# Kernel optimization log

Hardware: AMD Instinct MI355X
Metric: run time of the kernel (lower is better)

## Reference

```python
import jax, jax.numpy as jnp
import numpy as np

B, S, D, H, E = 2, 2048, 1024, 4096, 8


def setup_inputs() -> dict:
    key = jax.random.key(0)
    k0, k1, k2, k3 = jax.random.split(key, 4)
    x = jax.random.normal(k0, (B, S, D), dtype=jnp.float32)
    router_w = jax.random.normal(k1, (E, D), dtype=jnp.float32) * 0.02   # Top2Router Linear weight [E, D]
    w1 = jax.random.normal(k2, (E, D, H), dtype=jnp.float32) * 0.02      # stacked fc1 weights (transposed: x @ w1[e])
    w2 = jax.random.normal(k3, (E, H, D), dtype=jnp.float32) * 0.02      # stacked fc2 weights
    return {"x": x, "router_w": router_w, "w1": w1, "w2": w2}


def reference(x, router_w, w1, w2):
    # x: [B, S, D] -> flatten tokens. Single-rank EP: all-to-all is identity,
    # microbatch split is a pure overlap trick, per-token math unchanged.
    b, s, d = x.shape
    e = router_w.shape[0]
    xf = x.reshape(-1, d)                                     # [T, D]
    # Top-2 router with renormalized gate weights
    probs = jax.nn.softmax(xf @ router_w.T, axis=-1)          # [T, E]
    topv, topi = jax.lax.top_k(probs, 2)                      # [T, 2]
    topv = topv / (topv.sum(axis=-1, keepdims=True) + 1e-9)
    # Combine weights per expert: cw[t,e] = sum_k topv[t,k] * [topi[t,k]==e]
    cw = (jax.nn.one_hot(topi, e, dtype=xf.dtype) * topv[..., None]).sum(axis=1)  # [T, E]
    # Expert MLPs (dense-over-experts reference for the grouped GEMM)
    h = jax.nn.gelu(jnp.einsum('td,edh->teh', xf, w1), approximate=False)  # [T, E, H]
    y = jnp.einsum('teh,ehd->ted', h, w2)                                   # [T, E, D]
    out = jnp.einsum('te,ted->td', cw, y)                                   # weighted combine (scatter-add equiv.)
    return out.reshape(b, s, d)
```

## Files before the change

kernel.cpp:

```cpp
#include <hip/hip_runtime.h>

#define T_TOK 4096
#define DIM   1024
#define HID   4096
#define NEXP  8
#define MAXROWS 9216

typedef unsigned short u16;
typedef __attribute__((ext_vector_type(8))) short short8;
typedef __attribute__((ext_vector_type(4))) float f32x4;
typedef __attribute__((ext_vector_type(4))) unsigned short u16x4;
typedef __attribute__((ext_vector_type(8))) unsigned short u16x8;

typedef __attribute__((address_space(3))) unsigned int lds_uint;
typedef const __attribute__((address_space(1))) unsigned int gbl_uint;

__device__ __forceinline__ u16 f2bf(float f) {
    union { float f; unsigned int u; } v; v.f = f;
    unsigned int r = v.u + 0x7fffu + ((v.u >> 16) & 1u);
    return (u16)(r >> 16);
}

__device__ __forceinline__ float gelu_f(float v) {
    float u = 1.5957691216f * (v + 0.044715f * v * v * v);
    float s = 1.0f / (1.0f + __expf(-u));
    return v * s;
}

__global__ __launch_bounds__(256)
void transpose_cast2(const float* __restrict__ w1, u16* __restrict__ w1t,
                     const float* __restrict__ w2, u16* __restrict__ w2t,
                     int* __restrict__ counts) {
    int b = blockIdx.x;
    if (b == 0 && threadIdx.x < NEXP) counts[threadIdx.x] = 0;
    const float* in; u16* out; int R, C, bx, by, e;
    if (b < 8192) {
        e = b >> 10; int t = b & 1023; bx = t & 63; by = t >> 6;
        in = w1; out = w1t; R = DIM; C = HID;
    } else {
        b -= 8192;
        e = b >> 10; int t = b & 1023; bx = t & 15; by = t >> 4;
        in = w2; out = w2t; R = HID; C = DIM;
    }
    __shared__ u16 t[64 * 68];
    size_t mo = (size_t)e * DIM * HID;
    const float* ip = in + mo;
    u16* op = out + mo;
    int c0 = bx * 64, r0 = by * 64;
    int tid = threadIdx.x;
#pragma unroll
    for (int j = 0; j < 4; ++j) {
        int id = tid + 256 * j;
        int r = id >> 4, cc = id & 15;
        f32x4 v = *(const f32x4*)(ip + (size_t)(r0 + r) * C + c0 + 4 * cc);
        u16x4 w; w.x = f2bf(v.x); w.y = f2bf(v.y); w.z = f2bf(v.z); w.w = f2bf(v.w);
        *(u16x4*)(t + r * 68 + 4 * cc) = w;
    }
    __syncthreads();
#pragma unroll
    for (int j = 0; j < 4; ++j) {
        int id = tid + 256 * j;
        int c = id >> 4, rj = id & 15;
        u16x4 o;
        o.x = t[(4 * rj + 0) * 68 + c];
        o.y = t[(4 * rj + 1) * 68 + c];
        o.z = t[(4 * rj + 2) * 68 + c];
        o.w = t[(4 * rj + 3) * 68 + c];
        *(u16x4*)(op + (size_t)(c0 + c) * R + r0 + 4 * rj) = o;
    }
}

__global__ __launch_bounds__(256)
void router_k(const float* __restrict__ x, const float* __restrict__ rw,
              int* __restrict__ counts, int* __restrict__ tE,
              int* __restrict__ tS, float* __restrict__ tG) {
    int wave = threadIdx.x >> 6, lane = threadIdx.x & 63;
    int t = blockIdx.x * 4 + wave;
    const float* xr = x + (size_t)t * DIM;
    float xv[16];
#pragma unroll
    for (int i = 0; i < 16; ++i) xv[i] = xr[lane + 64*i];
    float lg[NEXP];
#pragma unroll
    for (int e = 0; e < NEXP; ++e) {
        const float* wr_ = rw + e * DIM;
        float a = 0.f;
#pragma unroll
        for (int i = 0; i < 16; ++i) a += xv[i] * wr_[lane + 64*i];
        lg[e] = a;
    }
#pragma unroll
    for (int off = 32; off > 0; off >>= 1)
#pragma unroll
        for (int e = 0; e < NEXP; ++e) lg[e] += __shfl_xor(lg[e], off, 64);
    if (lane == 0) {
        float mx = lg[0];
        for (int e = 1; e < NEXP; ++e) mx = fmaxf(mx, lg[e]);
        float p[NEXP], s = 0.f;
        for (int e = 0; e < NEXP; ++e) { p[e] = expf(lg[e] - mx); s += p[e]; }
        float inv_s = 1.f / s;
        for (int e = 0; e < NEXP; ++e) p[e] *= inv_s;
        int i0 = 0;
        for (int e = 1; e < NEXP; ++e) if (p[e] > p[i0]) i0 = e;
        int i1 = (i0 == 0) ? 1 : 0;
        for (int e = 0; e < NEXP; ++e) if (e != i0 && p[e] > p[i1]) i1 = e;
        float v0 = p[i0], v1 = p[i1];
        float inv = 1.f / (v0 + v1 + 1e-9f);
        int s0 = atomicAdd(&counts[i0], 1);
        int s1 = atomicAdd(&counts[i1], 1);
        tE[2*t] = i0;  tE[2*t+1] = i1;
        tS[2*t] = s0;  tS[2*t+1] = s1;
        tG[2*t] = v0 * inv;  tG[2*t+1] = v1 * inv;
    }
}

__device__ __forceinline__ int pbase_of(const int* __restrict__ counts, int e) {
    int pb = 0;
#pragma unroll
    for (int i = 0; i < NEXP; ++i) {
        int pad = ((counts[i] + 127) >> 7) << 7;
        pb += (i < e) ? pad : 0;
    }
    return pb;
}

__global__ __launch_bounds__(256)
void gather_k(const float* __restrict__ x, const int* __restrict__ tE,
              const int* __restrict__ tS, const int* __restrict__ counts,
              u16* __restrict__ xg) {
    int a = blockIdx.x;
    int t = a >> 1, k = a & 1;
    int e = tE[2*t + k];
    int row = pbase_of(counts, e) + tS[2*t + k];
    const f32x4* xr = (const f32x4*)(x + (size_t)t * DIM);
    u16x4* o = (u16x4*)(xg + (size_t)row * DIM);
    int i = threadIdx.x;
    f32x4 v = xr[i];
    u16x4 r; r.x = f2bf(v.x); r.y = f2bf(v.y); r.z = f2bf(v.z); r.w = f2bf(v.w);
    o[i] = r;
}

template<int K, int KSPLIT, bool GELU, typename OutT>
__global__ __launch_bounds__(256)
void gemm_bt(const u16* __restrict__ A, const u16* __restrict__ BtAll,
             OutT* __restrict__ C, const int* __restrict__ counts,
             int N, size_t cstride) {
    int e  = blockIdx.z / KSPLIT;
    int ks = blockIdx.z % KSPLIT;
    int cnt = counts[e];
    int mt = blockIdx.y;
    if (mt * 128 >= cnt) return;
    int row0 = pbase_of(counts, e) + mt * 128;
    const u16* Bt = BtAll + (size_t)e * N * K;
    OutT* Cp = C + (size_t)ks * cstride;
    int col0 = blockIdx.x * 128;
    const int kb0 = ks * (K / KSPLIT);
    constexpr int KITER = K / KSPLIT / 64;

    __shared__ __align__(16) u16 smem[128 * 128];
    u16* As = smem;
    u16* Bs = smem + 128 * 64;

    int tid = threadIdx.x;
    int lane = tid & 63;
    int w = tid >> 6;
    int quad = lane >> 4, m16 = lane & 15;
    int wr = (w >> 1) * 64, wc = (w & 1) * 64;
    int rsub = lane >> 3;
    int kch  = lane & 7;
    int kchs = kch ^ rsub;

    const u16* ga[4];
    const u16* gb[4];
#pragma unroll
    for (int i = 0; i < 4; ++i) {
        int r = (w * 4 + i) * 8 + rsub;
        ga[i] = A  + (size_t)(row0 + r) * K + kb0 + kchs * 8;
        gb[i] = Bt + (size_t)(col0 + r) * K + kb0 + kchs * 8;
    }
    int sw = m16 & 7;
    const u16* aP0 = As + (wr + m16) * 64 + ((quad       ^ sw) << 3);
    const u16* aP1 = As + (wr + m16) * 64 + (((4 + quad) ^ sw) << 3);
    const u16* bP0 = Bs + (wc + m16) * 64 + ((quad       ^ sw) << 3);
    const u16* bP1 = Bs + (wc + m16) * 64 + (((4 + quad) ^ sw) << 3);

    f32x4 acc[4][4] = {};

    for (int kit = 0; kit < KITER; ++kit) {
#pragma unroll
        for (int i = 0; i < 4; ++i) {
            int grp = w * 4 + i;
            __builtin_amdgcn_global_load_lds((gbl_uint*)ga[i], (lds_uint*)(As + grp * 512), 16, 0, 0);
            __builtin_amdgcn_global_load_lds((gbl_uint*)gb[i], (lds_uint*)(Bs + grp * 512), 16, 0, 0);
            ga[i] += 64; gb[i] += 64;
        }
        __syncthreads();
        {
            short8 af[4], bfr[4];
#pragma unroll
            for (int mi = 0; mi < 4; ++mi) af[mi]  = *(const short8*)(aP0 + mi * 1024);
#pragma unroll
            for (int ni = 0; ni < 4; ++ni) bfr[ni] = *(const short8*)(bP0 + ni * 1024);
#pragma unroll
            for (int mi = 0; mi < 4; ++mi)
#pragma unroll
                for (int ni = 0; ni < 4; ++ni)
                    acc[mi][ni] = __builtin_amdgcn_mfma_f32_16x16x32_bf16(af[mi], bfr[ni], acc[mi][ni], 0, 0, 0);
#pragma unroll
            for (int mi = 0; mi < 4; ++mi) af[mi]  = *(const short8*)(aP1 + mi * 1024);
#pragma unroll
            for (int ni = 0; ni < 4; ++ni) bfr[ni] = *(const short8*)(bP1 + ni * 1024);
#pragma unroll
            for (int mi = 0; mi < 4; ++mi)
#pragma unroll
                for (int ni = 0; ni < 4; ++ni)
                    acc[mi][ni] = __builtin_amdgcn_mfma_f32_16x16x32_bf16(af[mi], bfr[ni], acc[mi][ni], 0, 0, 0);
        }
        __syncthreads();
    }

    if (GELU) {
#pragma unroll
        for (int mi = 0; mi < 4; ++mi) {
#pragma unroll
            for (int r = 0; r < 4; ++r) {
                int row = wr + mi * 16 + quad * 4 + r;
#pragma unroll
                for (int ni = 0; ni < 4; ++ni) {
                    int col = wc + ni * 16 + m16;
                    int c16 = col >> 3, w8 = col & 7;
                    smem[row * 128 + (((c16 ^ (row & 15)) << 3) | w8)] = f2bf(gelu_f(acc[mi][ni][r]));
                }
            }
        }
        __syncthreads();
        int row_b = tid >> 4, c16_b = tid & 15;
        const u16* ls = smem + row_b * 128 + (((c16_b ^ (row_b & 15)) << 3));
        u16* gp = (u16*)Cp + (size_t)(row0 + row_b) * N + col0 + c16_b * 8;
#pragma unroll
        for (int j = 0; j < 8; ++j) {
            *(u16x8*)gp = *(const u16x8*)ls;
            ls += 16 * 128;
            gp += (size_t)16 * N;
        }
    } else {
        float* gp = (float*)Cp + (size_t)(row0 + wr + quad * 4) * N + col0 + wc + m16;
#pragma unroll
        for (int mi = 0; mi < 4; ++mi)
#pragma unroll
            for (int r = 0; r < 4; ++r) {
                float* rp = gp + (size_t)(mi * 16 + r) * N;
#pragma unroll
                for (int ni = 0; ni < 4; ++ni)
                    rp[ni * 16] = acc[mi][ni][r];
            }
    }
}

__global__ __launch_bounds__(256)
void combine_k(const float* __restrict__ p0, const float* __restrict__ p1,
               const int* __restrict__ tE, const int* __restrict__ tS,
               const float* __restrict__ tG, const int* __restrict__ counts,
               float* __restrict__ out) {
    int t = blockIdx.x;
    int e0 = tE[2*t], e1 = tE[2*t+1];
    int r0 = pbase_of(counts, e0) + tS[2*t];
    int r1 = pbase_of(counts, e1) + tS[2*t+1];
    float g0 = tG[2*t], g1 = tG[2*t+1];
    int i = threadIdx.x;
    f32x4 a0 = ((const f32x4*)(p0 + (size_t)r0 * DIM))[i];
    f32x4 b0 = ((const f32x4*)(p1 + (size_t)r0 * DIM))[i];
    f32x4 a1 = ((const f32x4*)(p0 + (size_t)r1 * DIM))[i];
    f32x4 b1 = ((const f32x4*)(p1 + (size_t)r1 * DIM))[i];
    f32x4* o = (f32x4*)(out + (size_t)t * DIM);
    o[i] = g0 * (a0 + b0) + g1 * (a1 + b1);
}

extern "C" void kernel_launch(void* const* d_in, const int* in_sizes, int n_in,
                              void* d_out, int out_size, void* d_ws, size_t ws_size,
                              hipStream_t stream) {
    const float* x  = (const float*)d_in[0];
    const float* rw = (const float*)d_in[1];
    const float* w1 = (const float*)d_in[2];
    const float* w2 = (const float*)d_in[3];
    float* out = (float*)d_out;

    char* ws = (char*)d_ws;
    u16* w1t = (u16*)(ws + 0);
    u16* xg  = (u16*)(ws + 67108864ull);
    u16* w2t = (u16*)(ws + 85983232ull);
    u16* hb  = (u16*)(ws + 153092096ull);
    float* p0 = (float*)(ws + 0);
    float* p1 = (float*)(ws + 37748736ull);
    int* ctrl   = (int*)(ws + 228589568ull);
    int* counts = ctrl;
    int* tE     = ctrl + 32;
    int* tS     = ctrl + 32 + 8192;
    float* tG   = (float*)(ctrl + 32 + 16384);

    transpose_cast2<<<16384, 256, 0, stream>>>(w1, w1t, w2, w2t, counts);
    router_k<<<T_TOK / 4, 256, 0, stream>>>(x, rw, counts, tE, tS, tG);
    gather_k<<<T_TOK * 2, 256, 0, stream>>>(x, tE, tS, counts, xg);
    gemm_bt<DIM, 1, true, u16><<<dim3(HID / 128, 32, NEXP), 256, 0, stream>>>(
        xg, w1t, hb, counts, HID, 0);
    gemm_bt<HID, 2, false, float><<<dim3(DIM / 128, 32, NEXP * 2), 256, 0, stream>>>(
        hb, w2t, p0, counts, DIM, (size_t)MAXROWS * DIM);
    combine_k<<<T_TOK, 256, 0, stream>>>(p0, p1, tE, tS, tG, counts, out);
}
```

Baseline: 671.5 us.

## Use 256x256 double-buffered 8-wave GEMM tiles and larger transpose tiles

Grows the grouped GEMM block tile from 128x128 to 256x256 with 512 threads. It double-buffers LDS so the next K-slab loads while MFMAs run, staged with barriers and s_setprio. Partial expert tiles are handled with row clamping and masked stores. The weight transpose-cast kernel moves to 128x128 tiles with 8-wide stores. The aim is more data reuse per LDS load and load/compute overlap, at the cost of more wasted work on partial tiles and 128KB of LDS per block, which limits occupancy.

Result: slower. 698.7 us (+4.1%).

```diff
diff --git a/kernel.cpp b/kernel.cpp
--- a/kernel.cpp
+++ b/kernel.cpp
@@ -9,6 +9,7 @@
 typedef unsigned short u16;
 typedef __attribute__((ext_vector_type(8))) short short8;
 typedef __attribute__((ext_vector_type(4))) float f32x4;
+typedef __attribute__((ext_vector_type(2))) unsigned short u16x2;
 typedef __attribute__((ext_vector_type(4))) unsigned short u16x4;
 typedef __attribute__((ext_vector_type(8))) unsigned short u16x8;
 
@@ -34,39 +35,39 @@
     int b = blockIdx.x;
     if (b == 0 && threadIdx.x < NEXP) counts[threadIdx.x] = 0;
     const float* in; u16* out; int R, C, bx, by, e;
-    if (b < 8192) {
-        e = b >> 10; int t = b & 1023; bx = t & 63; by = t >> 6;
+    if (b < 2048) {
+        e = b >> 8; int t = b & 255; bx = t & 31; by = t >> 5;
         in = w1; out = w1t; R = DIM; C = HID;
     } else {
-        b -= 8192;
-        e = b >> 10; int t = b & 1023; bx = t & 15; by = t >> 4;
+        b -= 2048;
+        e = b >> 8; int t = b & 255; bx = t & 7; by = t >> 3;
         in = w2; out = w2t; R = HID; C = DIM;
     }
-    __shared__ u16 t[64 * 68];
+    __shared__ u16 tl[128 * 130];
     size_t mo = (size_t)e * DIM * HID;
     const float* ip = in + mo;
     u16* op = out + mo;
-    int c0 = bx * 64, r0 = by * 64;
+    int c0 = bx * 128, r0 = by * 128;
     int tid = threadIdx.x;
 #pragma unroll
-    for (int j = 0; j < 4; ++j) {
+    for (int j = 0; j < 16; ++j) {
         int id = tid + 256 * j;
-        int r = id >> 4, cc = id & 15;
-        f32x4 v = *(const f32x4*)(ip + (size_t)(r0 + r) * C + c0 + 4 * cc);
-        u16x4 w; w.x = f2bf(v.x); w.y = f2bf(v.y); w.z = f2bf(v.z); w.w = f2bf(v.w);
-        *(u16x4*)(t + r * 68 + 4 * cc) = w;
+        int r = id >> 5, cg = id & 31;
+        f32x4 v = *(const f32x4*)(ip + (size_t)(r0 + r) * C + c0 + 4 * cg);
+        u16x2 wa; wa.x = f2bf(v.x); wa.y = f2bf(v.y);
+        u16x2 wb; wb.x = f2bf(v.z); wb.y = f2bf(v.w);
+        *(u16x2*)(tl + r * 130 + 4 * cg)     = wa;
+        *(u16x2*)(tl + r * 130 + 4 * cg + 2) = wb;
     }
     __syncthreads();
 #pragma unroll
-    for (int j = 0; j < 4; ++j) {
+    for (int j = 0; j < 8; ++j) {
         int id = tid + 256 * j;
-        int c = id >> 4, rj = id & 15;
-        u16x4 o;
-        o.x = t[(4 * rj + 0) * 68 + c];
-        o.y = t[(4 * rj + 1) * 68 + c];
-        o.z = t[(4 * rj + 2) * 68 + c];
-        o.w = t[(4 * rj + 3) * 68 + c];
-        *(u16x4*)(op + (size_t)(c0 + c) * R + r0 + 4 * rj) = o;
+        int c = id >> 4, ch = id & 15;
+        u16x8 o;
+#pragma unroll
+        for (int k = 0; k < 8; ++k) o[k] = tl[(ch * 8 + k) * 130 + c];
+        *(u16x8*)(op + (size_t)(c0 + c) * R + r0 + ch * 8) = o;
     }
 }
 
@@ -141,7 +142,7 @@
 }
 
 template<int K, int KSPLIT, bool GELU, typename OutT>
-__global__ __launch_bounds__(256)
+__global__ __launch_bounds__(512, 2)
 void gemm_bt(const u16* __restrict__ A, const u16* __restrict__ BtAll,
              OutT* __restrict__ C, const int* __restrict__ counts,
              int N, size_t cstride) {
@@ -149,23 +150,22 @@
     int ks = blockIdx.z % KSPLIT;
     int cnt = counts[e];
     int mt = blockIdx.y;
-    if (mt * 128 >= cnt) return;
-    int row0 = pbase_of(counts, e) + mt * 128;
+    if (mt * 256 >= cnt) return;
+    int row0 = pbase_of(counts, e) + mt * 256;
+    int limit = cnt - mt * 256;
     const u16* Bt = BtAll + (size_t)e * N * K;
     OutT* Cp = C + (size_t)ks * cstride;
-    int col0 = blockIdx.x * 128;
+    int col0 = blockIdx.x * 256;
     const int kb0 = ks * (K / KSPLIT);
-    constexpr int KITER = K / KSPLIT / 64;
-
-    __shared__ __align__(16) u16 smem[128 * 128];
-    u16* As = smem;
-    u16* Bs = smem + 128 * 64;
+    constexpr int NT = K / KSPLIT / 64;
+
+    __shared__ __align__(16) u16 smem[65536];
 
     int tid = threadIdx.x;
     int lane = tid & 63;
     int w = tid >> 6;
     int quad = lane >> 4, m16 = lane & 15;
-    int wr = (w >> 1) * 64, wc = (w & 1) * 64;
+    int wr = (w >> 2) * 128, wc = (w & 3) * 64;
     int rsub = lane >> 3;
     int kch  = lane & 7;
     int kchs = kch ^ rsub;
@@ -174,85 +174,151 @@
     const u16* gb[4];
 #pragma unroll
     for (int i = 0; i < 4; ++i) {
-        int r = (w * 4 + i) * 8 + rsub;
-        ga[i] = A  + (size_t)(row0 + r) * K + kb0 + kchs * 8;
-        gb[i] = Bt + (size_t)(col0 + r) * K + kb0 + kchs * 8;
+        int g = (w << 2) + i;
+        int ra = row0 + g * 8 + rsub;
+        if (ra > MAXROWS - 1) ra = MAXROWS - 1;
+        ga[i] = A  + (size_t)ra * K + kb0 + kchs * 8;
+        gb[i] = Bt + (size_t)(col0 + g * 8 + rsub) * K + kb0 + kchs * 8;
     }
     int sw = m16 & 7;
-    const u16* aP0 = As + (wr + m16) * 64 + ((quad       ^ sw) << 3);
-    const u16* aP1 = As + (wr + m16) * 64 + (((4 + quad) ^ sw) << 3);
-    const u16* bP0 = Bs + (wc + m16) * 64 + ((quad       ^ sw) << 3);
-    const u16* bP1 = Bs + (wc + m16) * 64 + (((4 + quad) ^ sw) << 3);
-
-    f32x4 acc[4][4] = {};
-
-    for (int kit = 0; kit < KITER; ++kit) {
-#pragma unroll
-        for (int i = 0; i < 4; ++i) {
-            int grp = w * 4 + i;
-            __builtin_amdgcn_global_load_lds((gbl_uint*)ga[i], (lds_uint*)(As + grp * 512), 16, 0, 0);
-            __builtin_amdgcn_global_load_lds((gbl_uint*)gb[i], (lds_uint*)(Bs + grp * 512), 16, 0, 0);
-            ga[i] += 64; gb[i] += 64;
-        }
-        __syncthreads();
-        {
-            short8 af[4], bfr[4];
-#pragma unroll
-            for (int mi = 0; mi < 4; ++mi) af[mi]  = *(const short8*)(aP0 + mi * 1024);
-#pragma unroll
-            for (int ni = 0; ni < 4; ++ni) bfr[ni] = *(const short8*)(bP0 + ni * 1024);
-#pragma unroll
-            for (int mi = 0; mi < 4; ++mi)
-#pragma unroll
-                for (int ni = 0; ni < 4; ++ni)
-                    acc[mi][ni] = __builtin_amdgcn_mfma_f32_16x16x32_bf16(af[mi], bfr[ni], acc[mi][ni], 0, 0, 0);
-#pragma unroll
-            for (int mi = 0; mi < 4; ++mi) af[mi]  = *(const short8*)(aP1 + mi * 1024);
-#pragma unroll
-            for (int ni = 0; ni < 4; ++ni) bfr[ni] = *(const short8*)(bP1 + ni * 1024);
-#pragma unroll
-            for (int mi = 0; mi < 4; ++mi)
-#pragma unroll
-                for (int ni = 0; ni < 4; ++ni)
-                    acc[mi][ni] = __builtin_amdgcn_mfma_f32_16x16x32_bf16(af[mi], bfr[ni], acc[mi][ni], 0, 0, 0);
-        }
-        __syncthreads();
+    const int aoff = (wr + m16) * 64;
+    const int boff = (wc + m16) * 64;
+    const int c0lo = (quad ^ sw) << 3;
+    const int c0hi = ((4 + quad) ^ sw) << 3;
+
+    f32x4 acc[8][4] = {};
+
+#pragma unroll
+    for (int i = 0; i < 4; ++i) {
+        int g = (w << 2) + i;
+        __builtin_amdgcn_global_load_lds((gbl_uint*)ga[i], (lds_uint*)(smem + g * 512), 16, 0, 0);
+        __builtin_amdgcn_global_load_lds((gbl_uint*)gb[i], (lds_uint*)(smem + 32768 + g * 512), 16, 0, 0);
+        ga[i] += 64; gb[i] += 64;
+    }
+    asm volatile("s_waitcnt vmcnt(0)" ::: "memory");
+    __builtin_amdgcn_s_barrier();
+
+#pragma unroll 2
+    for (int t = 0; t < NT; ++t) {
+        const u16* Ab = smem + (t & 1) * 16384;
+        const u16* Bb = smem + 32768 + (t & 1) * 16384;
+        short8 a0[4], a1[4], b0[4], b1[4];
+        if (t + 1 < NT) {
+#pragma unroll
+            for (int i = 0; i < 4; ++i) {
+                int g = (w << 2) + i;
+                __builtin_amdgcn_global_load_lds((gbl_uint*)ga[i],
+                    (lds_uint*)(smem + ((t + 1) & 1) * 16384 + g * 512), 16, 0, 0);
+                __builtin_amdgcn_global_load_lds((gbl_uint*)gb[i],
+                    (lds_uint*)(smem + 32768 + ((t + 1) & 1) * 16384 + g * 512), 16, 0, 0);
+                ga[i] += 64; gb[i] += 64;
+            }
+        }
+#pragma unroll
+        for (int m = 0; m < 4; ++m) {
+            a0[m] = *(const short8*)(Ab + aoff + m * 1024 + c0lo);
+            a1[m] = *(const short8*)(Ab + aoff + m * 1024 + c0hi);
+        }
+#pragma unroll
+        for (int n = 0; n < 2; ++n) {
+            b0[n] = *(const short8*)(Bb + boff + n * 1024 + c0lo);
+            b1[n] = *(const short8*)(Bb + boff + n * 1024 + c0hi);
+        }
+        __builtin_amdgcn_s_barrier();
+        asm volatile("s_waitcnt lgkmcnt(0)" ::: "memory");
+        __builtin_amdgcn_s_setprio(1);
+#pragma unroll
+        for (int m = 0; m < 4; ++m)
+#pragma unroll
+            for (int n = 0; n < 2; ++n) {
+                acc[m][n] = __builtin_amdgcn_mfma_f32_16x16x32_bf16(a0[m], b0[n], acc[m][n], 0, 0, 0);
+                acc[m][n] = __builtin_amdgcn_mfma_f32_16x16x32_bf16(a1[m], b1[n], acc[m][n], 0, 0, 0);
+            }
+        __builtin_amdgcn_s_setprio(0);
+        __builtin_amdgcn_s_barrier();
+#pragma unroll
+        for (int n = 2; n < 4; ++n) {
+            b0[n] = *(const short8*)(Bb + boff + n * 1024 + c0lo);
+            b1[n] = *(const short8*)(Bb + boff + n * 1024 + c0hi);
+        }
+        __builtin_amdgcn_s_barrier();
+        asm volatile("s_waitcnt lgkmcnt(0)" ::: "memory");
+        __builtin_amdgcn_s_setprio(1);
+#pragma unroll
+        for (int m = 0; m < 4; ++m)
+#pragma unroll
+            for (int n = 2; n < 4; ++n) {
+                acc[m][n] = __builtin_amdgcn_mfma_f32_16x16x32_bf16(a0[m], b0[n], acc[m][n], 0, 0, 0);
+                acc[m][n] = __builtin_amdgcn_mfma_f32_16x16x32_bf16(a1[m], b1[n], acc[m][n], 0, 0, 0);
+            }
+        __builtin_amdgcn_s_setprio(0);
+        __builtin_amdgcn_s_barrier();
+#pragma unroll
+        for (int m = 0; m < 4; ++m) {
+            a0[m] = *(const short8*)(Ab + aoff + (4 + m) * 1024 + c0lo);
+            a1[m] = *(const short8*)(Ab + aoff + (4 + m) * 1024 + c0hi);
+        }
+        __builtin_amdgcn_s_barrier();
+        asm volatile("s_waitcnt lgkmcnt(0)" ::: "memory");
+        __builtin_amdgcn_s_setprio(1);
+#pragma unroll
+        for (int m = 0; m < 4; ++m)
+#pragma unroll
+            for (int n = 2; n < 4; ++n) {
+                acc[4 + m][n] = __builtin_amdgcn_mfma_f32_16x16x32_bf16(a0[m], b0[n], acc[4 + m][n], 0, 0, 0);
+                acc[4 + m][n] = __builtin_amdgcn_mfma_f32_16x16x32_bf16(a1[m], b1[n], acc[4 + m][n], 0, 0, 0);
+            }
+        __builtin_amdgcn_s_setprio(0);
+        __builtin_amdgcn_s_barrier();
+        __builtin_amdgcn_s_setprio(1);
+#pragma unroll
+        for (int m = 0; m < 4; ++m)
+#pragma unroll
+            for (int n = 0; n < 2; ++n) {
+                acc[4 + m][n] = __builtin_amdgcn_mfma_f32_16x16x32_bf16(a0[m], b0[n], acc[4 + m][n], 0, 0, 0);
+                acc[4 + m][n] = __builtin_amdgcn_mfma_f32_16x16x32_bf16(a1[m], b1[n], acc[4 + m][n], 0, 0, 0);
+            }
+        __builtin_amdgcn_s_setprio(0);
+        asm volatile("s_waitcnt vmcnt(0)" ::: "memory");
+        __builtin_amdgcn_s_barrier();
     }
 
     if (GELU) {
 #pragma unroll
-        for (int mi = 0; mi < 4; ++mi) {
+        for (int mi = 0; mi < 8; ++mi) {
 #pragma unroll
             for (int r = 0; r < 4; ++r) {
                 int row = wr + mi * 16 + quad * 4 + r;
 #pragma unroll
                 for (int ni = 0; ni < 4; ++ni) {
                     int col = wc + ni * 16 + m16;
-                    int c16 = col >> 3, w8 = col & 7;
-                    smem[row * 128 + (((c16 ^ (row & 15)) << 3) | w8)] = f2bf(gelu_f(acc[mi][ni][r]));
+                    int ch = col >> 3, w8 = col & 7;
+                    smem[row * 256 + (((ch ^ (row & 31)) << 3) | w8)] = f2bf(gelu_f(acc[mi][ni][r]));
                 }
             }
         }
         __syncthreads();
-        int row_b = tid >> 4, c16_b = tid & 15;
-        const u16* ls = smem + row_b * 128 + (((c16_b ^ (row_b & 15)) << 3));
-        u16* gp = (u16*)Cp + (size_t)(row0 + row_b) * N + col0 + c16_b * 8;
-#pragma unroll
-        for (int j = 0; j < 8; ++j) {
-            *(u16x8*)gp = *(const u16x8*)ls;
-            ls += 16 * 128;
-            gp += (size_t)16 * N;
+        int rr = tid >> 5, ch = tid & 31;
+#pragma unroll
+        for (int it = 0; it < 16; ++it) {
+            int row = it * 16 + rr;
+            if (row < limit) {
+                u16x8 v = *(const u16x8*)(smem + row * 256 + ((ch ^ (row & 31)) << 3));
+                *(u16x8*)((u16*)Cp + (size_t)(row0 + row) * N + col0 + ch * 8) = v;
+            }
         }
     } else {
-        float* gp = (float*)Cp + (size_t)(row0 + wr + quad * 4) * N + col0 + wc + m16;
-#pragma unroll
-        for (int mi = 0; mi < 4; ++mi)
+#pragma unroll
+        for (int mi = 0; mi < 8; ++mi)
 #pragma unroll
             for (int r = 0; r < 4; ++r) {
-                float* rp = gp + (size_t)(mi * 16 + r) * N;
-#pragma unroll
-                for (int ni = 0; ni < 4; ++ni)
-                    rp[ni * 16] = acc[mi][ni][r];
+                int rl = wr + mi * 16 + quad * 4 + r;
+                if (rl < limit) {
+                    float* rp = (float*)Cp + (size_t)(row0 + rl) * N + col0 + wc + m16;
+#pragma unroll
+                    for (int ni = 0; ni < 4; ++ni)
+                        rp[ni * 16] = acc[mi][ni][r];
+                }
             }
     }
 }
@@ -298,12 +364,12 @@
     int* tS     = ctrl + 32 + 8192;
     float* tG   = (float*)(ctrl + 32 + 16384);
 
-    transpose_cast2<<<16384, 256, 0, stream>>>(w1, w1t, w2, w2t, counts);
+    transpose_cast2<<<4096, 256, 0, stream>>>(w1, w1t, w2, w2t, counts);
     router_k<<<T_TOK / 4, 256, 0, stream>>>(x, rw, counts, tE, tS, tG);
     gather_k<<<T_TOK * 2, 256, 0, stream>>>(x, tE, tS, counts, xg);
-    gemm_bt<DIM, 1, true, u16><<<dim3(HID / 128, 32, NEXP), 256, 0, stream>>>(
+    gemm_bt<DIM, 1, true, u16><<<dim3(HID / 256, 16, NEXP), 512, 0, stream>>>(
         xg, w1t, hb, counts, HID, 0);
-    gemm_bt<HID, 2, false, float><<<dim3(DIM / 128, 32, NEXP * 2), 256, 0, stream>>>(
+    gemm_bt<HID, 2, false, float><<<dim3(DIM / 256, 16, NEXP * 2), 512, 0, stream>>>(
         hb, w2t, p0, counts, DIM, (size_t)MAXROWS * DIM);
     combine_k<<<T_TOK, 256, 0, stream>>>(p0, p1, tE, tS, tG, counts, out);
 }
```
